# Kernel optimization log

Measured on AMD Instinct MI355X. Metric: run time of the kernel, lower is better.

Reference implementation:

```python
import jax, jax.numpy as jnp
import numpy as np
from functools import partial

IMG, P, C, E, DEPTH, H, FE, NCLS = 224, 16, 3, 768, 12, 12, 4, 1000
B = 32
NP = (IMG // P) ** 2          # 196 patches
N = NP + 1                    # +cls token
HD = E // H                   # 64
FF = FE * E                   # 3072
EPS = 1e-5


def setup_inputs() -> dict:
    key = jax.random.key(0)
    ks = iter(jax.random.split(key, 32))
    r = lambda shape, s=0.02: (jax.random.normal(next(ks), shape, jnp.float32) * s)
    inp = {
        "x": jax.random.normal(next(ks), (B, C, IMG, IMG), jnp.float32),
        "conv_w": r((E, C, P, P)),              # OIHW
        "conv_b": r((E,)),
        "cls_token": r((1, 1, E)),
        "pos_emb": r((1, N, E)),
        # stacked per-layer params; Linear weights stored as [in, out]
        "Wq": r((DEPTH, E, E)), "Wk": r((DEPTH, E, E)), "Wv": r((DEPTH, E, E)),
        "Wo": r((DEPTH, E, E)), "bo": r((DEPTH, E)),
        "ln1_g": jnp.ones((DEPTH, E)), "ln1_b": jnp.zeros((DEPTH, E)),
        "W1": r((DEPTH, E, FF)), "b1": r((DEPTH, FF)),
        "W2": r((DEPTH, FF, E)), "b2": r((DEPTH, E)),
        "ln2_g": jnp.ones((DEPTH, E)), "ln2_b": jnp.zeros((DEPTH, E)),
        "head_g": jnp.ones((E,)), "head_b": jnp.zeros((E,)),
        "head_W": r((E, NCLS)), "head_bias": r((NCLS,)),
    }
    return inp


def _ln(x, g, b):
    m = jnp.mean(x, axis=-1, keepdims=True)
    v = jnp.var(x, axis=-1, keepdims=True)
    return (x - m) * jax.lax.rsqrt(v + EPS) * g + b


def _block(h, p):
    Wq, Wk, Wv, Wo, bo, g1, bn1, W1, b1, W2, b2, g2, bn2 = p
    b, n, _ = h.shape
    q = (h @ Wq).reshape(b, n, H, HD)
    k = (h @ Wk).reshape(b, n, H, HD)
    v = (h @ Wv).reshape(b, n, H, HD)
    # NOTE: original scales by sqrt(embed_size), not sqrt(head_dim)
    energy = jnp.einsum("bqhd,bkhd->bhqk", q, k) / jnp.sqrt(jnp.float32(E))
    attn = jax.nn.softmax(energy, axis=-1)
    out = jnp.einsum("bhqk,bkhd->bqhd", attn, v).reshape(b, n, E)
    out = out @ Wo + bo
    x = _ln(out + h, g1, bn1)
    f = jax.nn.relu(x @ W1 + b1) @ W2 + b2
    return _ln(f + x, g2, bn2), None


def reference(x, conv_w, conv_b, cls_token, pos_emb, Wq, Wk, Wv, Wo, bo,
              ln1_g, ln1_b, W1, b1, W2, b2, ln2_g, ln2_b,
              head_g, head_b, head_W, head_bias):
    # patch embedding: strided conv == non-overlapping patch projection
    h = jax.lax.conv_general_dilated(
        x, conv_w, window_strides=(P, P), padding="VALID",
        dimension_numbers=("NCHW", "OIHW", "NCHW"))
    h = h + conv_b[None, :, None, None]
    h = h.reshape(B, E, NP).transpose(0, 2, 1)          # [B, NP, E]
    cls = jnp.broadcast_to(cls_token, (B, 1, E))
    h = jnp.concatenate([cls, h], axis=1) + pos_emb      # [B, N, E]
    params = (Wq, Wk, Wv, Wo, bo, ln1_g, ln1_b, W1, b1, W2, b2, ln2_g, ln2_b)
    h, _ = jax.lax.scan(_block, h, params)
    cls_final = h[:, 0]
    return _ln(cls_final, head_g, head_b) @ head_W + head_bias
```

## Files before the change

kernel.cpp:

```cpp
#include <hip/hip_runtime.h>

#define NTOK 197
#define BATCH 32
#define ROWS (BATCH*NTOK)
#define EMB 768
#define FFDIM 3072
#define NHEAD 12
#define HDIM 64
#define NPAD 224

typedef __bf16 bf16x8_t __attribute__((ext_vector_type(8)));
typedef float f32x4 __attribute__((ext_vector_type(4)));
typedef unsigned short u16;

__device__ __forceinline__ u16 f2b(float f) {
  union { float f; unsigned int u; } v; v.f = f;
  unsigned int r = v.u + 0x7fffu + ((v.u >> 16) & 1u);
  return (u16)(r >> 16);
}
__device__ __forceinline__ void gload16(const void* g, void* l) {
  __builtin_amdgcn_global_load_lds((const __attribute__((address_space(1))) void*)g,
                                   (__attribute__((address_space(3))) void*)l, 16, 0, 0);
}
__device__ __forceinline__ float wred_sum(float v) {
#pragma unroll
  for (int o = 32; o > 0; o >>= 1) v += __shfl_xor(v, o);
  return v;
}

template <bool HAS_BIAS, bool RELU, bool ADD_RES, bool OUT_BF16>
__global__ __launch_bounds__(256)
void gemm_bt(const u16* __restrict__ A, const u16* __restrict__ Bt, void* __restrict__ C,
             const float* __restrict__ bias, const float* __restrict__ res,
             int M, int N, int K) {
  __shared__ __align__(16) char lds[2][16384];
  const int tid = threadIdx.x;
  const int lane = tid & 63;
  const int wid = tid >> 6;
  const int wm = wid >> 1, wn = wid & 1;
  const int bm = blockIdx.y * 128, bn = blockIdx.x * 128;
  const int r15 = lane & 15, khi = lane >> 4;

  f32x4 acc[4][4] = {};
  const int nk = K >> 5;

  auto stage = [&](int buf, int kt) {
    const int k0 = kt * 32 + khi * 8;
#pragma unroll
    for (int i = 0; i < 4; ++i) {
      int s = wid * 4 + i;
      char* ldst = &lds[buf][s * 1024];
      const u16* g;
      if (s < 8) {
        int row = bm + s * 16 + r15; if (row >= M) row = M - 1;
        g = A + (size_t)row * K + k0;
      } else {
        int row = bn + (s - 8) * 16 + r15;
        g = Bt + (size_t)row * K + k0;
      }
      gload16(g, ldst);
    }
  };

  stage(0, 0);
  __syncthreads();
  for (int kt = 0; kt < nk; ++kt) {
    const int cur = kt & 1;
    if (kt + 1 < nk) stage(cur ^ 1, kt + 1);
    bf16x8_t a[4], b[4];
#pragma unroll
    for (int mt = 0; mt < 4; ++mt)
      a[mt] = *(const bf16x8_t*)&lds[cur][(wm * 4 + mt) * 1024 + lane * 16];
#pragma unroll
    for (int nt = 0; nt < 4; ++nt)
      b[nt] = *(const bf16x8_t*)&lds[cur][8192 + (wn * 4 + nt) * 1024 + lane * 16];
#pragma unroll
    for (int mt = 0; mt < 4; ++mt)
#pragma unroll
      for (int nt = 0; nt < 4; ++nt)
        acc[mt][nt] = __builtin_amdgcn_mfma_f32_16x16x32_bf16(a[mt], b[nt], acc[mt][nt], 0, 0, 0);
    __syncthreads();
  }

#pragma unroll
  for (int mt = 0; mt < 4; ++mt) {
#pragma unroll
    for (int nt = 0; nt < 4; ++nt) {
      const int col = bn + wn * 64 + nt * 16 + r15;
      float bv = 0.f;
      if (HAS_BIAS) bv = bias[col];
#pragma unroll
      for (int j = 0; j < 4; ++j) {
        const int row = bm + wm * 64 + mt * 16 + khi * 4 + j;
        if (row < M) {
          float v = acc[mt][nt][j] + bv;
          if (ADD_RES) v += res[(size_t)row * N + col];
          if (RELU) v = v > 0.f ? v : 0.f;
          if (OUT_BF16) ((u16*)C)[(size_t)row * N + col] = f2b(v);
          else          ((float*)C)[(size_t)row * N + col] = v;
        }
      }
    }
  }
}

__global__ __launch_bounds__(256)
void gemm_bt_sk(const u16* __restrict__ A, const u16* __restrict__ Bt,
                float* __restrict__ P0, float* __restrict__ P1,
                int M, int N, int K) {
  __shared__ __align__(16) char lds[2][16384];
  const int tid = threadIdx.x;
  const int lane = tid & 63;
  const int wid = tid >> 6;
  const int wm = wid >> 1, wn = wid & 1;
  const int bm = blockIdx.y * 128, bn = blockIdx.x * 128;
  const int r15 = lane & 15, khi = lane >> 4;
  const int Kh = K >> 1;
  const int kbase = blockIdx.z * Kh;
  float* __restrict__ C = blockIdx.z ? P1 : P0;

  f32x4 acc[4][4] = {};
  const int nk = Kh >> 5;

  auto stage = [&](int buf, int kt) {
    const int k0 = kbase + kt * 32 + khi * 8;
#pragma unroll
    for (int i = 0; i < 4; ++i) {
      int s = wid * 4 + i;
      char* ldst = &lds[buf][s * 1024];
      const u16* g;
      if (s < 8) {
        int row = bm + s * 16 + r15; if (row >= M) row = M - 1;
        g = A + (size_t)row * K + k0;
      } else {
        int row = bn + (s - 8) * 16 + r15;
        g = Bt + (size_t)row * K + k0;
      }
      gload16(g, ldst);
    }
  };

  stage(0, 0);
  __syncthreads();
  for (int kt = 0; kt < nk; ++kt) {
    const int cur = kt & 1;
    if (kt + 1 < nk) stage(cur ^ 1, kt + 1);
    bf16x8_t a[4], b[4];
#pragma unroll
    for (int mt = 0; mt < 4; ++mt)
      a[mt] = *(const bf16x8_t*)&lds[cur][(wm * 4 + mt) * 1024 + lane * 16];
#pragma unroll
    for (int nt = 0; nt < 4; ++nt)
      b[nt] = *(const bf16x8_t*)&lds[cur][8192 + (wn * 4 + nt) * 1024 + lane * 16];
#pragma unroll
    for (int mt = 0; mt < 4; ++mt)
#pragma unroll
      for (int nt = 0; nt < 4; ++nt)
        acc[mt][nt] = __builtin_amdgcn_mfma_f32_16x16x32_bf16(a[mt], b[nt], acc[mt][nt], 0, 0, 0);
    __syncthreads();
  }

#pragma unroll
  for (int mt = 0; mt < 4; ++mt) {
#pragma unroll
    for (int nt = 0; nt < 4; ++nt) {
      const int col = bn + wn * 64 + nt * 16 + r15;
#pragma unroll
      for (int j = 0; j < 4; ++j) {
        const int row = bm + wm * 64 + mt * 16 + khi * 4 + j;
        if (row < M) C[(size_t)row * N + col] = acc[mt][nt][j];
      }
    }
  }
}

__global__ __launch_bounds__(256)
void ln_red(const float* __restrict__ P0, const float* __restrict__ P1,
            const float* __restrict__ bias, const float* __restrict__ res,
            const float* __restrict__ g, const float* __restrict__ bv,
            float* __restrict__ o32, u16* __restrict__ obf) {
  const int row = blockIdx.x;
  const size_t base = (size_t)row * EMB;
  const int tid = threadIdx.x;
  float vv[3];
#pragma unroll
  for (int c = 0; c < 3; ++c) {
    int e = tid + c * 256;
    vv[c] = P0[base + e] + P1[base + e] + bias[e] + res[base + e];
  }
  float s = wred_sum(vv[0] + vv[1] + vv[2]);
  float s2 = wred_sum(vv[0] * vv[0] + vv[1] * vv[1] + vv[2] * vv[2]);
  __shared__ float rs[4], rq[4];
  const int wid = tid >> 6, lane = tid & 63;
  if (lane == 0) { rs[wid] = s; rq[wid] = s2; }
  __syncthreads();
  float S1 = rs[0] + rs[1] + rs[2] + rs[3];
  float S2 = rq[0] + rq[1] + rq[2] + rq[3];
  float mean = S1 * (1.0f / 768.0f);
  float var = S2 * (1.0f / 768.0f) - mean * mean;
  float inv = rsqrtf(var + 1e-5f);
#pragma unroll
  for (int c = 0; c < 3; ++c) {
    int e = tid + c * 256;
    float y = (vv[c] - mean) * inv * g[e] + bv[e];
    o32[base + e] = y;
    obf[base + e] = f2b(y);
  }
}

__global__ void prep_layer(const float* __restrict__ Wq, const float* __restrict__ Wk,
                           const float* __restrict__ Wv, const float* __restrict__ Wo,
                           const float* __restrict__ W1, const float* __restrict__ W2,
                           u16* __restrict__ qkvT, u16* __restrict__ woT,
                           u16* __restrict__ w1T, u16* __restrict__ w2T) {
  __shared__ float tbuf[32][33];
  const int t = blockIdx.x;
  const float* src; u16* dst; int K, N, nt, kt;
  if (t < 2304) {
    int seg = t / 576, r = t % 576;
    nt = r % 24; kt = r / 24; K = 768; N = 768;
    if (seg == 0)      { src = Wq; dst = qkvT; }
    else if (seg == 1) { src = Wk; dst = qkvT + (size_t)768 * 768; }
    else if (seg == 2) { src = Wv; dst = qkvT + (size_t)2 * 768 * 768; }
    else               { src = Wo; dst = woT; }
  } else if (t < 4608) {
    int r = t - 2304; nt = r % 96; kt = r / 96;
    K = 768; N = 3072; src = W1; dst = w1T;
  } else {
    int r = t - 4608; nt = r % 24; kt = r / 24;
    K = 3072; N = 768; src = W2; dst = w2T;
  }
  const int n0 = nt * 32, k0 = kt * 32;
  const int tx = threadIdx.x, ty = threadIdx.y;
#pragma unroll
  for (int i = 0; i < 4; ++i)
    tbuf[ty + i * 8][tx] = src[(size_t)(k0 + ty + i * 8) * N + n0 + tx];
  __syncthreads();
#pragma unroll
  for (int i = 0; i < 4; ++i)
    dst[(size_t)(n0 + ty + i * 8) * K + k0 + tx] = f2b(tbuf[tx][ty + i * 8]);
}

__global__ void convert_bf(const float* __restrict__ s, u16* __restrict__ d, size_t n) {
  size_t i = (size_t)blockIdx.x * 256 + threadIdx.x;
  if (i < n) d[i] = f2b(s[i]);
}

__global__ void transpose_head(const float* __restrict__ src, float* __restrict__ dst) {
  __shared__ float tbuf[32][33];
  const int n0 = blockIdx.x * 32, k0 = blockIdx.y * 32;
  const int tx = threadIdx.x, ty = threadIdx.y;
#pragma unroll
  for (int i = 0; i < 4; ++i) {
    int k = k0 + ty + i * 8, n = n0 + tx;
    if (n < 1000) tbuf[ty + i * 8][tx] = src[(size_t)k * 1000 + n];
  }
  __syncthreads();
#pragma unroll
  for (int i = 0; i < 4; ++i) {
    int n = n0 + ty + i * 8, k = k0 + tx;
    if (n < 1000) dst[(size_t)n * 768 + k] = tbuf[tx][ty + i * 8];
  }
}

__global__ void im2col(const float* __restrict__ x, u16* __restrict__ A) {
  size_t idx = (size_t)blockIdx.x * 256 + threadIdx.x;
  if (idx >= (size_t)6272 * 768) return;
  int k = (int)(idx % 768); size_t row = idx / 768;
  int b = (int)(row / 196), p = (int)(row % 196);
  int py = p / 14, px = p % 14;
  int c = k >> 8, rem = k & 255, ph = rem >> 4, pw = rem & 15;
  float v = x[(((size_t)b * 3 + c) * 224 + (py * 16 + ph)) * 224 + (px * 16 + pw)];
  A[idx] = f2b(v);
}

__global__ void assemble_h0(const float* __restrict__ pout, const float* __restrict__ cls,
                            const float* __restrict__ pos, float* __restrict__ h32,
                            u16* __restrict__ hbf) {
  const int row = blockIdx.x;
  const int b = row / NTOK, n = row % NTOK;
  for (int c = threadIdx.x; c < EMB; c += 256) {
    float v;
    if (n == 0) v = cls[c] + pos[c];
    else v = pout[((size_t)b * 196 + (n - 1)) * EMB + c] + pos[(size_t)n * EMB + c];
    h32[(size_t)row * EMB + c] = v;
    hbf[(size_t)row * EMB + c] = f2b(v);
  }
}

__global__ void build_vT(const u16* __restrict__ qkv, u16* __restrict__ vT) {
  size_t idx = (size_t)blockIdx.x * 256 + threadIdx.x;
  if (idx >= (size_t)384 * HDIM * NPAD) return;
  int nn = (int)(idx % NPAD); size_t t = idx / NPAD;
  int d = (int)(t % HDIM); int bh = (int)(t / HDIM);
  int b = bh / NHEAD, h = bh % NHEAD;
  u16 v = 0;
  if (nn < NTOK) v = qkv[((size_t)b * NTOK + nn) * 2304 + 1536 + h * HDIM + d];
  vT[idx] = v;
}

__global__ __launch_bounds__(256)
void attn_sm(const u16* __restrict__ qkv, u16* __restrict__ P) {
  __shared__ __align__(16) char kf[13 * 2 * 1024];
  __shared__ __align__(16) char qf[2 * 2 * 1024];
  __shared__ float S[32][NPAD];
  const int bh = blockIdx.y;
  const int b = bh / NHEAD, h = bh % NHEAD;
  const int qb = blockIdx.x;
  const int tid = threadIdx.x, lane = tid & 63, wid = tid >> 6;
  const int r15 = lane & 15, khi = lane >> 4;

  const u16* qbase = qkv + (size_t)b * NTOK * 2304 + h * HDIM;
  const u16* kbase = qbase + 768;

  for (int i = wid; i < 26; i += 4) {
    int sub = i >> 1, ks = i & 1;
    int row = sub * 16 + r15; if (row > 196) row = 196;
    gload16(kbase + (size_t)row * 2304 + ks * 32 + khi * 8, &kf[(size_t)i * 1024]);
  }
  {
    int i = wid;
    int sub = i >> 1, ks = i & 1;
    int row = qb * 32 + sub * 16 + r15; if (row > 196) row = 196;
    gload16(qbase + (size_t)row * 2304 + ks * 32 + khi * 8, &qf[(size_t)i * 1024]);
  }
  __syncthreads();

  const float scale = 0.03608439182435161f;
  for (int t = wid; t < 26; t += 4) {
    int qi = t / 13, ki = t % 13;
    f32x4 acc = {};
    bf16x8_t aq0 = *(const bf16x8_t*)&qf[(qi * 2 + 0) * 1024 + lane * 16];
    bf16x8_t aq1 = *(const bf16x8_t*)&qf[(qi * 2 + 1) * 1024 + lane * 16];
    bf16x8_t bk0 = *(const bf16x8_t*)&kf[(ki * 2 + 0) * 1024 + lane * 16];
    bf16x8_t bk1 = *(const bf16x8_t*)&kf[(ki * 2 + 1) * 1024 + lane * 16];
    acc = __builtin_amdgcn_mfma_f32_16x16x32_bf16(aq0, bk0, acc, 0, 0, 0);
    acc = __builtin_amdgcn_mfma_f32_16x16x32_bf16(aq1, bk1, acc, 0, 0, 0);
#pragma unroll
    for (int j = 0; j < 4; ++j) S[qi * 16 + khi * 4 + j][ki * 16 + r15] = acc[j] * scale;
  }
  __syncthreads();

  for (int i = 0; i < 8; ++i) {
    const int r = wid * 8 + i;
    const int q = qb * 32 + r;
    if (q > 196) continue;
    float vals[4]; float m = -1e30f;
#pragma unroll
    for (int c = 0; c < 4; ++c) {
      int col = lane + c * 64;
      float v = (col < NTOK) ? S[r][col] : -1e30f;
      vals[c] = v; m = fmaxf(m, v);
    }
#pragma unroll
    for (int o = 32; o > 0; o >>= 1) m = fmaxf(m, __shfl_xor(m, o));
    float s = 0.f;
#pragma unroll
    for (int c = 0; c < 4; ++c) { float e = __expf(vals[c] - m); vals[c] = e; s += e; }
    s = wred_sum(s);
    float inv = 1.f / s;
    u16* prow = P + ((size_t)bh * NTOK + q) * NPAD;
#pragma unroll
    for (int c = 0; c < 4; ++c) {
      int col = lane + c * 64;
      if (col < NPAD) prow[col] = f2b(vals[c] * inv);
    }
  }
}

__global__ __launch_bounds__(256)
void attn_pv(const u16* __restrict__ P, const u16* __restrict__ vT, u16* __restrict__ out) {
  __shared__ __align__(16) char lds[2][17 * 1024];
  const int bh = blockIdx.x;
  const int b = bh / NHEAD, h = bh % NHEAD;
  const int tid = threadIdx.x, lane = tid & 63, wid = tid >> 6;
  const int r15 = lane & 15, khi = lane >> 4;
  const u16* Pb = P + (size_t)bh * NTOK * NPAD;
  const u16* Vb = vT + (size_t)bh * HDIM * NPAD;

  f32x4 acc[4][4] = {};
  auto stage = [&](int buf, int kt) {
    for (int i = wid; i < 17; i += 4) {
      const u16* g;
      if (i < 13) { int row = i * 16 + r15; if (row > 196) row = 196;
                    g = Pb + (size_t)row * NPAD + kt * 32 + khi * 8; }
      else        { int row = (i - 13) * 16 + r15;
                    g = Vb + (size_t)row * NPAD + kt * 32 + khi * 8; }
      gload16(g, &lds[buf][i * 1024]);
    }
  };
  stage(0, 0);
  __syncthreads();
  for (int kt = 0; kt < 7; ++kt) {
    const int cur = kt & 1;
    if (kt + 1 < 7) stage(cur ^ 1, kt + 1);
    bf16x8_t bb[4];
#pragma unroll
    for (int di = 0; di < 4; ++di)
      bb[di] = *(const bf16x8_t*)&lds[cur][(13 + di) * 1024 + lane * 16];
#pragma unroll
    for (int s = 0; s < 4; ++s) {
      int qi = wid + s * 4;
      if (qi < 13) {
        bf16x8_t a = *(const bf16x8_t*)&lds[cur][qi * 1024 + lane * 16];
#pragma unroll
        for (int di = 0; di < 4; ++di)
          acc[s][di] = __builtin_amdgcn_mfma_f32_16x16x32_bf16(a, bb[di], acc[s][di], 0, 0, 0);
      }
    }
    __syncthreads();
  }
#pragma unroll
  for (int s = 0; s < 4; ++s) {
    int qi = wid + s * 4;
    if (qi >= 13) continue;
#pragma unroll
    for (int di = 0; di < 4; ++di) {
      int col = h * HDIM + di * 16 + r15;
#pragma unroll
      for (int j = 0; j < 4; ++j) {
        int q = qi * 16 + khi * 4 + j;
        if (q < NTOK) out[((size_t)b * NTOK + q) * EMB + col] = f2b(acc[s][di][j]);
      }
    }
  }
}

__global__ __launch_bounds__(256)
void ln_cls(const float* __restrict__ h32, const float* __restrict__ hg,
            const float* __restrict__ hb, float* __restrict__ cls_ln) {
  const int b = blockIdx.x;
  const float* xr = h32 + (size_t)b * NTOK * EMB;
  const int tid = threadIdx.x;
  float v0 = xr[tid], v1 = xr[tid + 256], v2 = xr[tid + 512];
  float s = wred_sum(v0 + v1 + v2);
  float s2 = wred_sum(v0 * v0 + v1 * v1 + v2 * v2);
  __shared__ float rs[4], rq[4];
  const int wid = tid >> 6, lane = tid & 63;
  if (lane == 0) { rs[wid] = s; rq[wid] = s2; }
  __syncthreads();
  float S1 = rs[0] + rs[1] + rs[2] + rs[3];
  float S2 = rq[0] + rq[1] + rq[2] + rq[3];
  float mean = S1 * (1.0f / 768.0f);
  float var = S2 * (1.0f / 768.0f) - mean * mean;
  float inv = rsqrtf(var + 1e-5f);
  cls_ln[(size_t)b * EMB + tid]       = (v0 - mean) * inv * hg[tid]       + hb[tid];
  cls_ln[(size_t)b * EMB + tid + 256] = (v1 - mean) * inv * hg[tid + 256] + hb[tid + 256];
  cls_ln[(size_t)b * EMB + tid + 512] = (v2 - mean) * inv * hg[tid + 512] + hb[tid + 512];
}

__global__ __launch_bounds__(256)
void head2(const float* __restrict__ cls_ln, const float* __restrict__ hWT,
           const float* __restrict__ bias, float* __restrict__ out) {
  __shared__ float t[EMB];
  const int b = blockIdx.y;
  const int tid = threadIdx.x, lane = tid & 63, wid = tid >> 6;
  t[tid] = cls_ln[(size_t)b * EMB + tid];
  t[tid + 256] = cls_ln[(size_t)b * EMB + tid + 256];
  t[tid + 512] = cls_ln[(size_t)b * EMB + tid + 512];
  __syncthreads();
  const int j = blockIdx.x * 4 + wid;
  const float* wr = hWT + (size_t)j * EMB;
  float a = 0.f;
#pragma unroll
  for (int i = 0; i < 12; ++i) {
    int e = lane + i * 64;
    a += t[e] * wr[e];
  }
  a = wred_sum(a);
  if (lane == 0) out[(size_t)b * 1000 + j] = a + bias[j];
}

extern "C" void kernel_launch(void* const* d_in, const int* in_sizes, int n_in,
                              void* d_out, int out_size, void* d_ws, size_t ws_size,
                              hipStream_t stream) {
  const float* x      = (const float*)d_in[0];
  const float* conv_w = (const float*)d_in[1];
  const float* conv_b = (const float*)d_in[2];
  const float* cls    = (const float*)d_in[3];
  const float* pos    = (const float*)d_in[4];
  const float* Wq     = (const float*)d_in[5];
  const float* Wk     = (const float*)d_in[6];
  const float* Wv     = (const float*)d_in[7];
  const float* Wo     = (const float*)d_in[8];
  const float* bo     = (const float*)d_in[9];
  const float* ln1g   = (const float*)d_in[10];
  const float* ln1b   = (const float*)d_in[11];
  const float* W1     = (const float*)d_in[12];
  const float* b1     = (const float*)d_in[13];
  const float* W2     = (const float*)d_in[14];
  const float* b2     = (const float*)d_in[15];
  const float* ln2g   = (const float*)d_in[16];
  const float* ln2b   = (const float*)d_in[17];
  const float* hg     = (const float*)d_in[18];
  const float* hb     = (const float*)d_in[19];
  const float* hW     = (const float*)d_in[20];
  const float* hbias  = (const float*)d_in[21];

  char* ws = (char*)d_ws;
  size_t off = 0;
  auto alloc = [&](size_t bytes) { void* p = ws + off; off += (bytes + 255) & ~(size_t)255; return p; };

  u16*   qkvT = (u16*)alloc((size_t)2304 * 768 * 2);
  u16*   woTl = (u16*)alloc((size_t)768 * 768 * 2);
  u16*   w1Tl = (u16*)alloc((size_t)3072 * 768 * 2);
  u16*   w2Tl = (u16*)alloc((size_t)768 * 3072 * 2);
  u16*   cw   = (u16*)alloc((size_t)768 * 768 * 2);
  float* h32  = (float*)alloc((size_t)ROWS * EMB * 4);
  u16*   hbf  = (u16*)alloc((size_t)ROWS * EMB * 2);
  u16*   qkv  = (u16*)alloc((size_t)ROWS * 2304 * 2);
  char*  big  = (char*)alloc((size_t)384 * NTOK * NPAD * 2 + (size_t)384 * HDIM * NPAD * 2);
  u16*   Pbuf = (u16*)big;
  u16*   vT   = (u16*)(big + (size_t)384 * NTOK * NPAD * 2);
  u16*   mid  = (u16*)big;
  float* pout = (float*)big;
  float* woP0 = (float*)big;
  float* woP1 = (float*)(big + (size_t)ROWS * EMB * 4);
  u16*   att  = (u16*)alloc((size_t)ROWS * EMB * 2);
  u16*   xbf  = att;
  float* ybuf = (float*)alloc((size_t)ROWS * EMB * 4);
  float* x32  = (float*)alloc((size_t)ROWS * EMB * 4);
  float* hWT  = (float*)alloc((size_t)1000 * EMB * 4);
  float* clsl = (float*)alloc((size_t)32 * EMB * 4);
  u16*   Apatch = qkv;
  float* f2P0 = (float*)qkv;
  float* f2P1 = ybuf;

  if (off > ws_size) return;

  convert_bf<<<2304, 256, 0, stream>>>(conv_w, cw, (size_t)768 * 768);
  transpose_head<<<dim3(32, 24), dim3(32, 8), 0, stream>>>(hW, hWT);
  im2col<<<18816, 256, 0, stream>>>(x, Apatch);
  gemm_bt<true, false, false, false><<<dim3(6, 49), 256, 0, stream>>>(Apatch, cw, pout, conv_b, nullptr, 6272, 768, 768);
  assemble_h0<<<ROWS, 256, 0, stream>>>(pout, cls, pos, h32, hbf);

  for (int l = 0; l < 12; ++l) {
    const size_t wo = (size_t)l * 768 * 768;
    prep_layer<<<6912, dim3(32, 8), 0, stream>>>(
        Wq + wo, Wk + wo, Wv + wo, Wo + wo,
        W1 + (size_t)l * 768 * 3072, W2 + (size_t)l * 3072 * 768,
        qkvT, woTl, w1Tl, w2Tl);
    gemm_bt<false, false, false, true><<<dim3(18, 50), 256, 0, stream>>>(
        hbf, qkvT, qkv, nullptr, nullptr, ROWS, 2304, 768);
    build_vT<<<21504, 256, 0, stream>>>(qkv, vT);
    attn_sm<<<dim3(7, 384), 256, 0, stream>>>(qkv, Pbuf);
    attn_pv<<<384, 256, 0, stream>>>(Pbuf, vT, att);
    gemm_bt_sk<<<dim3(6, 50, 2), 256, 0, stream>>>(att, woTl, woP0, woP1, ROWS, 768, 768);
    ln_red<<<ROWS, 256, 0, stream>>>(woP0, woP1, bo + (size_t)l * 768, h32,
                                     ln1g + (size_t)l * 768, ln1b + (size_t)l * 768, x32, xbf);
    gemm_bt<true, true, false, true><<<dim3(24, 50), 256, 0, stream>>>(
        xbf, w1Tl, mid, b1 + (size_t)l * 3072, nullptr, ROWS, FFDIM, 768);
    gemm_bt_sk<<<dim3(6, 50, 2), 256, 0, stream>>>(mid, w2Tl, f2P0, f2P1, ROWS, 768, FFDIM);
    ln_red<<<ROWS, 256, 0, stream>>>(f2P0, f2P1, b2 + (size_t)l * 768, x32,
                                     ln2g + (size_t)l * 768, ln2b + (size_t)l * 768, h32, hbf);
  }

  ln_cls<<<32, 256, 0, stream>>>(h32, hg, hb, clsl);
  head2<<<dim3(250, 32), 256, 0, stream>>>(clsl, hWT, hbias, (float*)d_out);
}
```

Before: 4.178 ms.

## Add XCD-aware block swizzle to GEMMs and split projection GEMMs three ways

Remaps workgroup IDs so consecutive output tiles land on the same XCD, aiming to improve L2 reuse of shared A/B tiles across the chiplets. The Wo and FFN2 split-K GEMMs now split K three ways instead of two, raising the block count from 600 to 900 to fill more CUs. The third partial buffer reuses existing scratch (ybuf, h32), and ln_red sums three partials. The cost is extra partial-sum traffic and aliasing of h32, which is read and written element-wise in the same ln_red call.

Result: no change. 4.173 ms (-0.1%).

```diff
diff --git a/kernel.cpp b/kernel.cpp
--- a/kernel.cpp
+++ b/kernel.cpp
@@ -28,6 +28,16 @@
   return v;
 }
 
+__device__ __forceinline__ void xcd_swz(int& bx, int& by) {
+  const int gx = gridDim.x;
+  const int nwg = gx * gridDim.y;
+  const int orig = by * gx + bx;
+  const int q = nwg >> 3, r = nwg & 7;
+  const int xcd = orig & 7, idx = orig >> 3;
+  const int wg = (xcd < r ? xcd * (q + 1) : r * (q + 1) + (xcd - r) * q) + idx;
+  by = wg / gx; bx = wg % gx;
+}
+
 template <bool HAS_BIAS, bool RELU, bool ADD_RES, bool OUT_BF16>
 __global__ __launch_bounds__(256)
 void gemm_bt(const u16* __restrict__ A, const u16* __restrict__ Bt, void* __restrict__ C,
@@ -38,7 +48,9 @@
   const int lane = tid & 63;
   const int wid = tid >> 6;
   const int wm = wid >> 1, wn = wid & 1;
-  const int bm = blockIdx.y * 128, bn = blockIdx.x * 128;
+  int bxs = blockIdx.x, bys = blockIdx.y;
+  xcd_swz(bxs, bys);
+  const int bm = bys * 128, bn = bxs * 128;
   const int r15 = lane & 15, khi = lane >> 4;
 
   f32x4 acc[4][4] = {};
@@ -104,20 +116,23 @@
   }
 }
 
+template <int NSK>
 __global__ __launch_bounds__(256)
 void gemm_bt_sk(const u16* __restrict__ A, const u16* __restrict__ Bt,
-                float* __restrict__ P0, float* __restrict__ P1,
+                float* __restrict__ P0, float* __restrict__ P1, float* __restrict__ P2,
                 int M, int N, int K) {
   __shared__ __align__(16) char lds[2][16384];
   const int tid = threadIdx.x;
   const int lane = tid & 63;
   const int wid = tid >> 6;
   const int wm = wid >> 1, wn = wid & 1;
-  const int bm = blockIdx.y * 128, bn = blockIdx.x * 128;
+  int bxs = blockIdx.x, bys = blockIdx.y;
+  xcd_swz(bxs, bys);
+  const int bm = bys * 128, bn = bxs * 128;
   const int r15 = lane & 15, khi = lane >> 4;
-  const int Kh = K >> 1;
+  const int Kh = K / NSK;
   const int kbase = blockIdx.z * Kh;
-  float* __restrict__ C = blockIdx.z ? P1 : P0;
+  float* __restrict__ C = (blockIdx.z == 0) ? P0 : (blockIdx.z == 1 ? P1 : P2);
 
   f32x4 acc[4][4] = {};
   const int nk = Kh >> 5;
@@ -176,6 +191,7 @@
 
 __global__ __launch_bounds__(256)
 void ln_red(const float* __restrict__ P0, const float* __restrict__ P1,
+            const float* __restrict__ P2,
             const float* __restrict__ bias, const float* __restrict__ res,
             const float* __restrict__ g, const float* __restrict__ bv,
             float* __restrict__ o32, u16* __restrict__ obf) {
@@ -186,7 +202,7 @@
 #pragma unroll
   for (int c = 0; c < 3; ++c) {
     int e = tid + c * 256;
-    vv[c] = P0[base + e] + P1[base + e] + bias[e] + res[base + e];
+    vv[c] = P0[base + e] + P1[base + e] + P2[base + e] + bias[e] + res[base + e];
   }
   float s = wred_sum(vv[0] + vv[1] + vv[2]);
   float s2 = wred_sum(vv[0] * vv[0] + vv[1] * vv[1] + vv[2] * vv[2]);
@@ -523,8 +539,10 @@
   float* hWT  = (float*)alloc((size_t)1000 * EMB * 4);
   float* clsl = (float*)alloc((size_t)32 * EMB * 4);
   u16*   Apatch = qkv;
+  float* woP2 = ybuf;
   float* f2P0 = (float*)qkv;
   float* f2P1 = ybuf;
+  float* f2P2 = h32;
 
   if (off > ws_size) return;
 
@@ -545,13 +563,13 @@
     build_vT<<<21504, 256, 0, stream>>>(qkv, vT);
     attn_sm<<<dim3(7, 384), 256, 0, stream>>>(qkv, Pbuf);
     attn_pv<<<384, 256, 0, stream>>>(Pbuf, vT, att);
-    gemm_bt_sk<<<dim3(6, 50, 2), 256, 0, stream>>>(att, woTl, woP0, woP1, ROWS, 768, 768);
-    ln_red<<<ROWS, 256, 0, stream>>>(woP0, woP1, bo + (size_t)l * 768, h32,
+    gemm_bt_sk<3><<<dim3(6, 50, 3), 256, 0, stream>>>(att, woTl, woP0, woP1, woP2, ROWS, 768, 768);
+    ln_red<<<ROWS, 256, 0, stream>>>(woP0, woP1, woP2, bo + (size_t)l * 768, h32,
                                      ln1g + (size_t)l * 768, ln1b + (size_t)l * 768, x32, xbf);
     gemm_bt<true, true, false, true><<<dim3(24, 50), 256, 0, stream>>>(
         xbf, w1Tl, mid, b1 + (size_t)l * 3072, nullptr, ROWS, FFDIM, 768);
-    gemm_bt_sk<<<dim3(6, 50, 2), 256, 0, stream>>>(mid, w2Tl, f2P0, f2P1, ROWS, 768, FFDIM);
-    ln_red<<<ROWS, 256, 0, stream>>>(f2P0, f2P1, b2 + (size_t)l * 768, x32,
+    gemm_bt_sk<3><<<dim3(6, 50, 3), 256, 0, stream>>>(mid, w2Tl, f2P0, f2P1, f2P2, ROWS, 768, FFDIM);
+    ln_red<<<ROWS, 256, 0, stream>>>(f2P0, f2P1, f2P2, b2 + (size_t)l * 768, x32,
                                      ln2g + (size_t)l * 768, ln2b + (size_t)l * 768, h32, hbf);
   }
 
```
